# Kernel tuning notes

Hardware: AMD Instinct MI355X
Metric: run time of the kernel (lower is better)

Reference implementation:

```python
import jax, jax.numpy as jnp
import numpy as np
from jax import lax

B, L, C_IN = 8, 4096, 9
D_MODEL, D_STATE, D_CONV, EXPAND, N_LAYERS = 128, 16, 4, 2, 2
D_INNER = EXPAND * D_MODEL
DT_RANK = (D_MODEL + 15) // 16  # 8, mamba default ceil(d_model/16)


def setup_inputs() -> dict:
    key = jax.random.key(0)
    ks = jax.random.split(key, 8)
    s = 0.02
    A_log = jnp.log(jnp.broadcast_to(
        jnp.arange(1, D_STATE + 1, dtype=jnp.float32), (N_LAYERS, D_INNER, D_STATE)))
    return {
        "t": jax.random.normal(ks[0], (B, L, C_IN), jnp.float32),
        "emb_w": jax.random.normal(ks[1], (D_MODEL, C_IN, 3), jnp.float32) * s,
        "in_proj_w": jax.random.normal(ks[2], (N_LAYERS, 2 * D_INNER, D_MODEL), jnp.float32) * s,
        "conv_w": jax.random.normal(ks[3], (N_LAYERS, D_INNER, D_CONV), jnp.float32) * s,
        "conv_b": jnp.zeros((N_LAYERS, D_INNER), jnp.float32),
        "x_proj_w": jax.random.normal(ks[4], (N_LAYERS, DT_RANK + 2 * D_STATE, D_INNER), jnp.float32) * s,
        "dt_proj_w": jax.random.normal(ks[5], (N_LAYERS, D_INNER, DT_RANK), jnp.float32) * (DT_RANK ** -0.5),
        "dt_proj_b": jnp.full((N_LAYERS, D_INNER), -4.6, jnp.float32),  # softplus^-1(~0.01)
        "A_log": A_log,
        "D": jnp.ones((N_LAYERS, D_INNER), jnp.float32),
        "out_proj_w": jax.random.normal(ks[6], (N_LAYERS, D_MODEL, D_INNER), jnp.float32) * s,
    }


def token_embed(t, w):
    # circular-padded Conv1d(c_in -> d_model, kernel=3, padding=1, bias=False)
    Lt = t.shape[1]
    xp = jnp.pad(t, ((0, 0), (1, 1), (0, 0)), mode="wrap")  # (B, L+2, c_in)
    out = jnp.zeros((t.shape[0], Lt, w.shape[0]), t.dtype)
    for k in range(3):
        out = out + jnp.einsum("blc,dc->bld", xp[:, k:k + Lt], w[:, :, k])
    return out


def selective_scan(u, dt, A, Bm, Cm, Dv):
    # u, dt: (B,L,d_in); Bm, Cm: (B,L,d_state); A: (d_in,d_state); Dv: (d_in,)
    h0 = jnp.zeros((u.shape[0], u.shape[2], A.shape[1]), u.dtype)

    def step(h, xs):
        dt_i, b_i, c_i, u_i = xs  # (B,d_in), (B,ds), (B,ds), (B,d_in)
        dA = jnp.exp(dt_i[..., None] * A)                      # (B,d_in,ds)
        h = dA * h + (dt_i * u_i)[..., None] * b_i[:, None, :]  # (B,d_in,ds)
        y = jnp.einsum("bds,bs->bd", h, c_i)
        return h, y

    _, ys = lax.scan(step, h0, (dt.swapaxes(0, 1), Bm.swapaxes(0, 1),
                                 Cm.swapaxes(0, 1), u.swapaxes(0, 1)))
    return ys.swapaxes(0, 1) + u * Dv  # (B,L,d_in)


def mamba_block(x, in_w, cw, cb, xp_w, dtw, dtb, A_log, Dv, ow):
    Lt = x.shape[1]
    xz = jnp.einsum("bld,ed->ble", x, in_w)            # (B,L,2*d_inner)
    xc, z = jnp.split(xz, 2, axis=-1)
    # causal depthwise conv1d (kernel d_conv) + bias + silu
    xpad = jnp.pad(xc, ((0, 0), (D_CONV - 1, 0), (0, 0)))
    conv = cb
    acc = jnp.zeros_like(xc)
    for k in range(D_CONV):
        acc = acc + xpad[:, k:k + Lt] * cw[:, k]
    xc = jax.nn.silu(acc + cb)
    # input-dependent dt, B, C
    dbl = jnp.einsum("bld,rd->blr", xc, xp_w)           # (B,L,dt_rank+2*ds)
    dt = dbl[..., :DT_RANK]
    Bm = dbl[..., DT_RANK:DT_RANK + D_STATE]
    Cm = dbl[..., DT_RANK + D_STATE:]
    dt = jax.nn.softplus(jnp.einsum("blr,dr->bld", dt, dtw) + dtb)
    A = -jnp.exp(A_log)
    y = selective_scan(xc, dt, A, Bm, Cm, Dv)
    y = y * jax.nn.silu(z)
    return jnp.einsum("bld,md->blm", y, ow)             # (B,L,d_model)


def reference(t, emb_w, in_proj_w, conv_w, conv_b, x_proj_w, dt_proj_w,
              dt_proj_b, A_log, D, out_proj_w):
    x = token_embed(t, emb_w)
    for i in range(N_LAYERS):
        x = mamba_block(x, in_proj_w[i], conv_w[i], conv_b[i], x_proj_w[i],
                        dt_proj_w[i], dt_proj_b[i], A_log[i], D[i], out_proj_w[i])
    pooled = x.mean(axis=1)  # AdaptiveAvgPool1d(1) over time + flatten -> (B, d_model)
    nrm = jnp.maximum(jnp.linalg.norm(pooled, axis=1, keepdims=True), 1e-12)
    return pooled / nrm
```

## Files before the change

kernel.cpp:

```cpp
#include <hip/hip_runtime.h>
#include <cmath>

#define LOG2E 1.4426950408889634f
#define LN2   0.6931471805599453f

constexpr int Bb = 8;
constexpr int Ll = 4096;
constexpr int Mrows = Bb * Ll;
constexpr int NC = 128;
constexpr int CL = Ll / NC;

__device__ __forceinline__ float hexp2(float x) { return __builtin_amdgcn_exp2f(x); }
__device__ __forceinline__ float hlog2(float x) { return __builtin_amdgcn_logf(x); }
__device__ __forceinline__ float hrcp(float x)  { return __builtin_amdgcn_rcpf(x); }

__device__ __forceinline__ float softplus_f(float x) {
  const float t = hexp2(-fabsf(x) * LOG2E);
  return fmaxf(x, 0.f) + LN2 * hlog2(1.f + t);
}
__device__ __forceinline__ float sigmoid_f(float x) {
  return hrcp(1.f + hexp2(-x * LOG2E));
}

__global__ __launch_bounds__(128) void k_embed(const float* __restrict__ t,
                                               const float* __restrict__ w,
                                               float* __restrict__ x) {
  __shared__ float ws[128 * 27];
  const int d = threadIdx.x;
  for (int i = d; i < 128 * 27; i += 128) ws[i] = w[i];
  __syncthreads();
  const int bpb = Ll / 32;
  const int b = blockIdx.x / bpb;
  const int l0 = (blockIdx.x % bpb) * 32;
  const float* wd = &ws[d * 27];
  for (int l = l0; l < l0 + 32; ++l) {
    float acc = 0.f;
#pragma unroll
    for (int k = 0; k < 3; ++k) {
      int li = l + k - 1;
      if (li < 0) li += Ll;
      if (li >= Ll) li -= Ll;
      const float* tr = t + ((size_t)b * Ll + li) * 9;
#pragma unroll
      for (int c = 0; c < 9; ++c) acc = fmaf(tr[c], wd[c * 3 + k], acc);
    }
    x[((size_t)b * Ll + l) * 128 + d] = acc;
  }
}

template <int BM, int BN, int BK, int TM, int TN>
__global__ __launch_bounds__(256) void sgemm_tn(const float* __restrict__ A, int lda,
                                                const float* __restrict__ W, int ldw,
                                                float* __restrict__ C, int ldc,
                                                int N, int K) {
  constexpr int TX = BN / TN;
  constexpr int TY = BM / TM;
  static_assert(TX * TY == 256, "bad tile");
  __shared__ float As[BK][BM + 4];
  __shared__ float Bs[BK][BN + 4];
  const int m0 = blockIdx.x * BM;
  const int n0 = blockIdx.y * BN;
  const int tid = threadIdx.x;
  const int tx = tid % TX, ty = tid / TX;
  float acc[TM][TN];
#pragma unroll
  for (int i = 0; i < TM; ++i)
#pragma unroll
    for (int j = 0; j < TN; ++j) acc[i][j] = 0.f;

  constexpr int KV = BK / 4;
  const int lrow = tid / KV;
  const int lcol = (tid % KV) * 4;
  constexpr int RSTEP = 256 / KV;

  for (int k0 = 0; k0 < K; k0 += BK) {
#pragma unroll
    for (int r = lrow; r < BM; r += RSTEP) {
      float4 v = *(const float4*)(A + (size_t)(m0 + r) * lda + k0 + lcol);
      As[lcol + 0][r] = v.x; As[lcol + 1][r] = v.y;
      As[lcol + 2][r] = v.z; As[lcol + 3][r] = v.w;
    }
#pragma unroll
    for (int r = lrow; r < BN; r += RSTEP) {
      float4 v = make_float4(0.f, 0.f, 0.f, 0.f);
      if (n0 + r < N) v = *(const float4*)(W + (size_t)(n0 + r) * ldw + k0 + lcol);
      Bs[lcol + 0][r] = v.x; Bs[lcol + 1][r] = v.y;
      Bs[lcol + 2][r] = v.z; Bs[lcol + 3][r] = v.w;
    }
    __syncthreads();
#pragma unroll
    for (int k = 0; k < BK; ++k) {
      float ra[TM], rb[TN];
#pragma unroll
      for (int i = 0; i < TM; i += 4) {
        float4 v = *(const float4*)&As[k][ty * TM + i];
        ra[i + 0] = v.x; ra[i + 1] = v.y; ra[i + 2] = v.z; ra[i + 3] = v.w;
      }
#pragma unroll
      for (int j = 0; j < TN; j += 4) {
        float4 v = *(const float4*)&Bs[k][tx * TN + j];
        rb[j + 0] = v.x; rb[j + 1] = v.y; rb[j + 2] = v.z; rb[j + 3] = v.w;
      }
#pragma unroll
      for (int i = 0; i < TM; ++i)
#pragma unroll
        for (int j = 0; j < TN; ++j) acc[i][j] = fmaf(ra[i], rb[j], acc[i][j]);
    }
    __syncthreads();
  }
#pragma unroll
  for (int i = 0; i < TM; ++i) {
    const size_t row = (size_t)(m0 + ty * TM + i) * ldc + n0;
#pragma unroll
    for (int j = 0; j < TN; j += 4) {
      const int col = tx * TN + j;
      if (n0 + col < N) {
        float4 v = make_float4(acc[i][j], acc[i][j + 1], acc[i][j + 2], acc[i][j + 3]);
        *(float4*)(C + row + col) = v;
      }
    }
  }
}

__global__ __launch_bounds__(256) void k_conv_silu(const float* __restrict__ xz,
                                                   const float* __restrict__ cw,
                                                   const float* __restrict__ cb,
                                                   float* __restrict__ u) {
  const int idx = blockIdx.x * 256 + threadIdx.x;
  const int d = idx & 255;
  const int bl = idx >> 8;
  const int l = bl & (Ll - 1);
  const float4 wv = *(const float4*)(cw + d * 4);
  float acc = 0.f;
  if (l >= 3) {
    acc = fmaf(xz[((size_t)(bl - 3)) * 512 + d], wv.x, acc);
    acc = fmaf(xz[((size_t)(bl - 2)) * 512 + d], wv.y, acc);
    acc = fmaf(xz[((size_t)(bl - 1)) * 512 + d], wv.z, acc);
    acc = fmaf(xz[((size_t)(bl - 0)) * 512 + d], wv.w, acc);
  } else {
    if (l >= 2) acc = fmaf(xz[((size_t)(bl - 2)) * 512 + d], wv.y, acc);
    if (l >= 1) acc = fmaf(xz[((size_t)(bl - 1)) * 512 + d], wv.z, acc);
    acc = fmaf(xz[((size_t)bl) * 512 + d], wv.w, acc);
  }
  acc += cb[d];
  u[idx] = acc * sigmoid_f(acc);
}

#define LOAD_A2(base)                                                        \
  float4 a2a = *(const float4*)((base));                                     \
  float4 a2b = *(const float4*)((base) + 4);                                 \
  float4 a2c = *(const float4*)((base) + 8);                                 \
  float4 a2d = *(const float4*)((base) + 12);                                \
  a2a.x = -expf(a2a.x) * LOG2E; a2a.y = -expf(a2a.y) * LOG2E;                \
  a2a.z = -expf(a2a.z) * LOG2E; a2a.w = -expf(a2a.w) * LOG2E;                \
  a2b.x = -expf(a2b.x) * LOG2E; a2b.y = -expf(a2b.y) * LOG2E;                \
  a2b.z = -expf(a2b.z) * LOG2E; a2b.w = -expf(a2b.w) * LOG2E;                \
  a2c.x = -expf(a2c.x) * LOG2E; a2c.y = -expf(a2c.y) * LOG2E;                \
  a2c.z = -expf(a2c.z) * LOG2E; a2c.w = -expf(a2c.w) * LOG2E;                \
  a2d.x = -expf(a2d.x) * LOG2E; a2d.y = -expf(a2d.y) * LOG2E;                \
  a2d.z = -expf(a2d.z) * LOG2E; a2d.w = -expf(a2d.w) * LOG2E;

#define DT_FROM_Q(q0, q1, w0, w1, dtbv)                                      \
  float dtr = (dtbv);                                                        \
  dtr = fmaf((q0).x, (w0).x, dtr); dtr = fmaf((q0).y, (w0).y, dtr);          \
  dtr = fmaf((q0).z, (w0).z, dtr); dtr = fmaf((q0).w, (w0).w, dtr);          \
  dtr = fmaf((q1).x, (w1).x, dtr); dtr = fmaf((q1).y, (w1).y, dtr);          \
  dtr = fmaf((q1).z, (w1).z, dtr); dtr = fmaf((q1).w, (w1).w, dtr);

#define UPD1(H, A, Bv)                                                       \
  (H).x = fmaf(hexp2(sp * (A).x), (H).x, dtu * (Bv).x);                      \
  (H).y = fmaf(hexp2(sp * (A).y), (H).y, dtu * (Bv).y);                      \
  (H).z = fmaf(hexp2(sp * (A).z), (H).z, dtu * (Bv).z);                      \
  (H).w = fmaf(hexp2(sp * (A).w), (H).w, dtu * (Bv).w);

#define UPD3(H, A, Bv, Cv)                                                   \
  (H).x = fmaf(hexp2(sp * (A).x), (H).x, dtu * (Bv).x);                      \
  y = fmaf((H).x, (Cv).x, y);                                                \
  (H).y = fmaf(hexp2(sp * (A).y), (H).y, dtu * (Bv).y);                      \
  y = fmaf((H).y, (Cv).y, y);                                                \
  (H).z = fmaf(hexp2(sp * (A).z), (H).z, dtu * (Bv).z);                      \
  y = fmaf((H).z, (Cv).z, y);                                                \
  (H).w = fmaf(hexp2(sp * (A).w), (H).w, dtu * (Bv).w);                      \
  y = fmaf((H).w, (Cv).w, y);

__global__ __launch_bounds__(256) void k_scan_ph1(
    const float* __restrict__ u, const float* __restrict__ dbl,
    const float* __restrict__ dtw, const float* __restrict__ dtb,
    const float* __restrict__ alog, float* __restrict__ hloc,
    float* __restrict__ sdtc) {
  const int b = blockIdx.x / NC;
  const int c = blockIdx.x % NC;
  const int d = threadIdx.x;
  LOAD_A2(alog + d * 16)
  const float4 w0 = *(const float4*)(dtw + d * 8);
  const float4 w1 = *(const float4*)(dtw + d * 8 + 4);
  const float dtbv = dtb[d];
  float4 ha = make_float4(0.f, 0.f, 0.f, 0.f);
  float4 hb = ha, hc = ha, hd = ha;
  float sdt = 0.f;
  const float* ub = u + (size_t)b * Ll * 256 + d;
  const float* db = dbl + (size_t)b * Ll * 40;
  const int l0 = c * CL;
  for (int l = l0; l < l0 + CL; ++l) {
    const float uv = ub[(size_t)l * 256];
    const float* dr = db + (size_t)l * 40;
    const float4 q0 = *(const float4*)(dr);
    const float4 q1 = *(const float4*)(dr + 4);
    const float4 bfa = *(const float4*)(dr + 8);
    const float4 bfb = *(const float4*)(dr + 12);
    const float4 bfc = *(const float4*)(dr + 16);
    const float4 bfd = *(const float4*)(dr + 20);
    DT_FROM_Q(q0, q1, w0, w1, dtbv)
    const float sp = softplus_f(dtr);
    sdt += sp;
    const float dtu = sp * uv;
    UPD1(ha, a2a, bfa)
    UPD1(hb, a2b, bfb)
    UPD1(hc, a2c, bfc)
    UPD1(hd, a2d, bfd)
  }
  const size_t o = (size_t)(b * NC + c) * 256 + d;
  *(float4*)(hloc + o * 16 + 0)  = ha;
  *(float4*)(hloc + o * 16 + 4)  = hb;
  *(float4*)(hloc + o * 16 + 8)  = hc;
  *(float4*)(hloc + o * 16 + 12) = hd;
  sdtc[o] = sdt;
}

__global__ __launch_bounds__(256) void k_scan_ph2(
    const float* __restrict__ alog, const float* __restrict__ hloc,
    const float* __restrict__ sdtc, float* __restrict__ hstart) {
  const int b = blockIdx.x >> 4;
  const int dg = blockIdx.x & 15;
  const int d = dg * 16 + (threadIdx.x >> 4);
  const int s = threadIdx.x & 15;
  const float A2 = -expf(alog[d * 16 + s]) * LOG2E;
  float hs = 0.f;
  for (int c = 0; c < NC; ++c) {
    const size_t o = (size_t)(b * NC + c) * 256 + d;
    hstart[o * 16 + s] = hs;
    const float sdt = sdtc[o];
    hs = fmaf(hexp2(A2 * sdt), hs, hloc[o * 16 + s]);
  }
}

__global__ __launch_bounds__(256) void k_scan_ph3(
    const float* __restrict__ u, const float* __restrict__ dbl,
    const float* __restrict__ dtw, const float* __restrict__ dtb,
    const float* __restrict__ alog, const float* __restrict__ Dv,
    const float* __restrict__ hstart, float* __restrict__ xz) {
  const int b = blockIdx.x / NC;
  const int c = blockIdx.x % NC;
  const int d = threadIdx.x;
  LOAD_A2(alog + d * 16)
  const float4 w0 = *(const float4*)(dtw + d * 8);
  const float4 w1 = *(const float4*)(dtw + d * 8 + 4);
  const float dtbv = dtb[d];
  const float Dd = Dv[d];
  const size_t o = (size_t)(b * NC + c) * 256 + d;
  float4 ha = *(const float4*)(hstart + o * 16 + 0);
  float4 hb = *(const float4*)(hstart + o * 16 + 4);
  float4 hc = *(const float4*)(hstart + o * 16 + 8);
  float4 hd = *(const float4*)(hstart + o * 16 + 12);
  const float* ub = u + (size_t)b * Ll * 256 + d;
  const float* db = dbl + (size_t)b * Ll * 40;
  const int l0 = c * CL;
  for (int l = l0; l < l0 + CL; ++l) {
    const float uv = ub[(size_t)l * 256];
    const float* dr = db + (size_t)l * 40;
    const float4 q0 = *(const float4*)(dr);
    const float4 q1 = *(const float4*)(dr + 4);
    const float4 bfa = *(const float4*)(dr + 8);
    const float4 bfb = *(const float4*)(dr + 12);
    const float4 bfc = *(const float4*)(dr + 16);
    const float4 bfd = *(const float4*)(dr + 20);
    const float4 cfa = *(const float4*)(dr + 24);
    const float4 cfb = *(const float4*)(dr + 28);
    const float4 cfc = *(const float4*)(dr + 32);
    const float4 cfd = *(const float4*)(dr + 36);
    DT_FROM_Q(q0, q1, w0, w1, dtbv)
    const float sp = softplus_f(dtr);
    const float dtu = sp * uv;
    float y = 0.f;
    UPD3(ha, a2a, bfa, cfa)
    UPD3(hb, a2b, bfb, cfb)
    UPD3(hc, a2c, bfc, cfc)
    UPD3(hd, a2d, bfd, cfd)
    y = fmaf(uv, Dd, y);
    const size_t row = ((size_t)b * Ll + l) * 512;
    const float zv = xz[row + 256 + d];
    xz[row + d] = y * (zv * sigmoid_f(zv));
  }
}

__global__ __launch_bounds__(128) void k_pool_part(const float* __restrict__ x,
                                                   float* __restrict__ part) {
  const int b = blockIdx.x >> 5;
  const int c = blockIdx.x & 31;
  const int m = threadIdx.x;
  const float* xb = x + (size_t)b * Ll * 128 + (size_t)c * 128 * 128 + m;
  float s = 0.f;
#pragma unroll 4
  for (int l = 0; l < 128; ++l) s += xb[(size_t)l * 128];
  part[(size_t)blockIdx.x * 128 + m] = s;
}

__global__ __launch_bounds__(128) void k_pool_fin(const float* __restrict__ part,
                                                  float* __restrict__ out) {
  const int b = blockIdx.x, m = threadIdx.x;
  float p = 0.f;
#pragma unroll
  for (int c = 0; c < 32; ++c) p += part[((size_t)b * 32 + c) * 128 + m];
  p *= (1.f / Ll);
  __shared__ float pm[128];
  __shared__ float sq[128];
  pm[m] = p;
  sq[m] = p * p;
  __syncthreads();
  for (int wd = 64; wd >= 1; wd >>= 1) {
    if (m < wd) sq[m] += sq[m + wd];
    __syncthreads();
  }
  out[b * 128 + m] = pm[m] / fmaxf(sqrtf(sq[0]), 1e-12f);
}

extern "C" void kernel_launch(void* const* d_in, const int* in_sizes, int n_in,
                              void* d_out, int out_size, void* d_ws, size_t ws_size,
                              hipStream_t stream) {
  (void)in_sizes; (void)n_in; (void)out_size; (void)ws_size;
  const float* t    = (const float*)d_in[0];
  const float* embw = (const float*)d_in[1];
  const float* inw  = (const float*)d_in[2];
  const float* cw   = (const float*)d_in[3];
  const float* cb   = (const float*)d_in[4];
  const float* xpw  = (const float*)d_in[5];
  const float* dtw  = (const float*)d_in[6];
  const float* dtb  = (const float*)d_in[7];
  const float* alog = (const float*)d_in[8];
  const float* Dv   = (const float*)d_in[9];
  const float* ow   = (const float*)d_in[10];

  float* wsf  = (float*)d_ws;
  float* xz   = wsf;
  float* xb   = xz + 16777216;
  float* ubuf = xb + 4194304;
  float* dblb = ubuf + 8388608;
  float* hloc = dblb + 1310720;
  float* hst  = hloc + 4194304;
  float* sdtc = hst + 4194304;
  float* pool = sdtc + 262144;
  float* outp = (float*)d_out;

  k_embed<<<dim3(Bb * (Ll / 32)), dim3(128), 0, stream>>>(t, embw, xb);

  for (int layer = 0; layer < 2; ++layer) {
    const float* inw_l = inw + (size_t)layer * 512 * 128;
    const float* cw_l  = cw + layer * 256 * 4;
    const float* cb_l  = cb + layer * 256;
    const float* xpw_l = xpw + layer * 40 * 256;
    const float* dtw_l = dtw + layer * 256 * 8;
    const float* dtb_l = dtb + layer * 256;
    const float* al_l  = alog + layer * 256 * 16;
    const float* D_l   = Dv + layer * 256;
    const float* ow_l  = ow + layer * 128 * 256;

    sgemm_tn<128, 128, 32, 8, 8><<<dim3(Mrows / 128, 4), 256, 0, stream>>>(
        xb, 128, inw_l, 128, xz, 512, 512, 128);
    k_conv_silu<<<dim3(Mrows), 256, 0, stream>>>(xz, cw_l, cb_l, ubuf);
    sgemm_tn<64, 64, 32, 4, 4><<<dim3(Mrows / 64, 1), 256, 0, stream>>>(
        ubuf, 256, xpw_l, 256, dblb, 40, 40, 256);
    k_scan_ph1<<<dim3(Bb * NC), 256, 0, stream>>>(ubuf, dblb, dtw_l, dtb_l, al_l, hloc, sdtc);
    k_scan_ph2<<<dim3(Bb * 16), 256, 0, stream>>>(al_l, hloc, sdtc, hst);
    k_scan_ph3<<<dim3(Bb * NC), 256, 0, stream>>>(ubuf, dblb, dtw_l, dtb_l, al_l, D_l, hst, xz);
    sgemm_tn<64, 128, 32, 4, 8><<<dim3(Mrows / 64, 1), 256, 0, stream>>>(
        xz, 512, ow_l, 256, xb, 128, 128, 256);
  }

  k_pool_part<<<dim3(Bb * 32), 128, 0, stream>>>(xb, pool);
  k_pool_fin<<<dim3(Bb), 128, 0, stream>>>(pool, outp);
}
```

Before: 479.7 us.

## Replace FP32 SIMT GEMMs with split-bf16 triple-MFMA GEMMs and drop hstart buffer

Replaces the three fp32 SIMT sgemm calls with an MFMA kernel that splits each fp32 operand into three bf16 pieces (hi/mid/lo) and combines six bf16 MFMAs to emulate near-fp32 accuracy. Weights are pre-split by new kernels on each call, and activations are split in-kernel while staging to LDS. The scan phase 2 now writes chunk start states in place into hloc, removing the separate hstart buffer. This trades more MFMA issues and split arithmetic for higher matrix throughput, and takes a small accuracy risk from the bf16 decomposition.

```diff
diff --git a/kernel.cpp b/kernel.cpp
--- a/kernel.cpp
+++ b/kernel.cpp
@@ -3,6 +3,7 @@
 
 #define LOG2E 1.4426950408889634f
 #define LN2   0.6931471805599453f
+#define C8    0.00390625f
 
 constexpr int Bb = 8;
 constexpr int Ll = 4096;
@@ -10,6 +11,10 @@
 constexpr int NC = 128;
 constexpr int CL = Ll / NC;
 
+typedef unsigned short u16;
+typedef short s16x8 __attribute__((ext_vector_type(8)));
+typedef float f32x4 __attribute__((ext_vector_type(4)));
+
 __device__ __forceinline__ float hexp2(float x) { return __builtin_amdgcn_exp2f(x); }
 __device__ __forceinline__ float hlog2(float x) { return __builtin_amdgcn_logf(x); }
 __device__ __forceinline__ float hrcp(float x)  { return __builtin_amdgcn_rcpf(x); }
@@ -20,6 +25,38 @@
 }
 __device__ __forceinline__ float sigmoid_f(float x) {
   return hrcp(1.f + hexp2(-x * LOG2E));
+}
+
+__device__ __forceinline__ f32x4 mfma_bf(s16x8 a, s16x8 b, f32x4 c) {
+  return __builtin_amdgcn_mfma_f32_16x16x32_bf16(a, b, c, 0, 0, 0);
+}
+
+__device__ __forceinline__ u16 bf16rne(float v) {
+  unsigned u = __float_as_uint(v);
+  u += 0x7FFFu + ((u >> 16) & 1u);
+  return (u16)(u >> 16);
+}
+__device__ __forceinline__ float bf2f(u16 h) {
+  return __uint_as_float(((unsigned)h) << 16);
+}
+__device__ __forceinline__ void split3(float v, u16& h, u16& m, u16& l) {
+  h = bf16rne(v);
+  const float r1 = (v - bf2f(h)) * 256.f;
+  m = bf16rne(r1);
+  const float r2 = (r1 - bf2f(m)) * 256.f;
+  l = bf16rne(r2);
+}
+
+__global__ __launch_bounds__(256) void k_split3(const float* __restrict__ src,
+                                                u16* __restrict__ h,
+                                                u16* __restrict__ m,
+                                                u16* __restrict__ l, int n) {
+  const int i = blockIdx.x * 256 + threadIdx.x;
+  if (i < n) {
+    u16 a, b, c;
+    split3(src[i], a, b, c);
+    h[i] = a; m[i] = b; l[i] = c;
+  }
 }
 
 __global__ __launch_bounds__(128) void k_embed(const float* __restrict__ t,
@@ -48,75 +85,101 @@
   }
 }
 
-template <int BM, int BN, int BK, int TM, int TN>
-__global__ __launch_bounds__(256) void sgemm_tn(const float* __restrict__ A, int lda,
-                                                const float* __restrict__ W, int ldw,
-                                                float* __restrict__ C, int ldc,
-                                                int N, int K) {
-  constexpr int TX = BN / TN;
-  constexpr int TY = BM / TM;
-  static_assert(TX * TY == 256, "bad tile");
-  __shared__ float As[BK][BM + 4];
-  __shared__ float Bs[BK][BN + 4];
-  const int m0 = blockIdx.x * BM;
-  const int n0 = blockIdx.y * BN;
+__global__ __launch_bounds__(512) void gemm3s(
+    const float* __restrict__ A, int lda,
+    const u16* __restrict__ Wh, const u16* __restrict__ Wm,
+    const u16* __restrict__ Wl,
+    float* __restrict__ C, int ldc, int N, int K) {
+  __shared__ __align__(16) u16 Lh[128 * 40];
+  __shared__ __align__(16) u16 Lm[128 * 40];
+  __shared__ __align__(16) u16 Ll2[128 * 40];
+  const int m0 = blockIdx.x * 128;
+  const int n0 = blockIdx.y * 128;
   const int tid = threadIdx.x;
-  const int tx = tid % TX, ty = tid / TX;
-  float acc[TM][TN];
-#pragma unroll
-  for (int i = 0; i < TM; ++i)
-#pragma unroll
-    for (int j = 0; j < TN; ++j) acc[i][j] = 0.f;
-
-  constexpr int KV = BK / 4;
-  const int lrow = tid / KV;
-  const int lcol = (tid % KV) * 4;
-  constexpr int RSTEP = 256 / KV;
-
-  for (int k0 = 0; k0 < K; k0 += BK) {
-#pragma unroll
-    for (int r = lrow; r < BM; r += RSTEP) {
-      float4 v = *(const float4*)(A + (size_t)(m0 + r) * lda + k0 + lcol);
-      As[lcol + 0][r] = v.x; As[lcol + 1][r] = v.y;
-      As[lcol + 2][r] = v.z; As[lcol + 3][r] = v.w;
+  const int lane = tid & 63;
+  const int wid = tid >> 6;
+  const int wm = wid & 1;
+  const int wn = wid >> 1;
+  const int lr = lane & 15;
+  const int lq = lane >> 4;
+
+  f32x4 a0[4][2], a1[4][2], a2[4][2];
+  const f32x4 zz = {0.f, 0.f, 0.f, 0.f};
+#pragma unroll
+  for (int i = 0; i < 4; ++i)
+#pragma unroll
+    for (int j = 0; j < 2; ++j) { a0[i][j] = zz; a1[i][j] = zz; a2[i][j] = zz; }
+
+  const int col0 = n0 + wn * 32 + lr;
+  const int col1 = col0 + 16;
+  const int c0 = col0 < N ? col0 : N - 1;
+  const int c1 = col1 < N ? col1 : N - 1;
+  const size_t bo0 = (size_t)c0 * K + lq * 8;
+  const size_t bo1 = (size_t)c1 * K + lq * 8;
+
+  const int srow = tid >> 2;
+  const int sg = (tid & 3) * 8;
+  const float* pa = A + (size_t)(m0 + srow) * lda + sg;
+  const int sdst = srow * 40 + sg;
+
+  for (int k0 = 0; k0 < K; k0 += 32) {
+    const float4 va = *(const float4*)(pa + k0);
+    const float4 vb = *(const float4*)(pa + k0 + 4);
+    s16x8 h8, m8, l8;
+    {
+      u16 h, m, l;
+      split3(va.x, h, m, l); h8[0] = (short)h; m8[0] = (short)m; l8[0] = (short)l;
+      split3(va.y, h, m, l); h8[1] = (short)h; m8[1] = (short)m; l8[1] = (short)l;
+      split3(va.z, h, m, l); h8[2] = (short)h; m8[2] = (short)m; l8[2] = (short)l;
+      split3(va.w, h, m, l); h8[3] = (short)h; m8[3] = (short)m; l8[3] = (short)l;
+      split3(vb.x, h, m, l); h8[4] = (short)h; m8[4] = (short)m; l8[4] = (short)l;
+      split3(vb.y, h, m, l); h8[5] = (short)h; m8[5] = (short)m; l8[5] = (short)l;
+      split3(vb.z, h, m, l); h8[6] = (short)h; m8[6] = (short)m; l8[6] = (short)l;
+      split3(vb.w, h, m, l); h8[7] = (short)h; m8[7] = (short)m; l8[7] = (short)l;
     }
-#pragma unroll
-    for (int r = lrow; r < BN; r += RSTEP) {
-      float4 v = make_float4(0.f, 0.f, 0.f, 0.f);
-      if (n0 + r < N) v = *(const float4*)(W + (size_t)(n0 + r) * ldw + k0 + lcol);
-      Bs[lcol + 0][r] = v.x; Bs[lcol + 1][r] = v.y;
-      Bs[lcol + 2][r] = v.z; Bs[lcol + 3][r] = v.w;
+    *(s16x8*)&Lh[sdst] = h8;
+    *(s16x8*)&Lm[sdst] = m8;
+    *(s16x8*)&Ll2[sdst] = l8;
+    __syncthreads();
+    const s16x8 bh0 = *(const s16x8*)(Wh + bo0 + k0);
+    const s16x8 bh1 = *(const s16x8*)(Wh + bo1 + k0);
+    const s16x8 bm0 = *(const s16x8*)(Wm + bo0 + k0);
+    const s16x8 bm1 = *(const s16x8*)(Wm + bo1 + k0);
+    const s16x8 bl0 = *(const s16x8*)(Wl + bo0 + k0);
+    const s16x8 bl1 = *(const s16x8*)(Wl + bo1 + k0);
+#pragma unroll
+    for (int mf = 0; mf < 4; ++mf) {
+      const int ar = (wm * 64 + mf * 16 + lr) * 40 + lq * 8;
+      const s16x8 ah = *(const s16x8*)&Lh[ar];
+      const s16x8 am = *(const s16x8*)&Lm[ar];
+      const s16x8 al = *(const s16x8*)&Ll2[ar];
+      a0[mf][0] = mfma_bf(ah, bh0, a0[mf][0]);
+      a1[mf][0] = mfma_bf(ah, bm0, a1[mf][0]);
+      a1[mf][0] = mfma_bf(am, bh0, a1[mf][0]);
+      a2[mf][0] = mfma_bf(ah, bl0, a2[mf][0]);
+      a2[mf][0] = mfma_bf(al, bh0, a2[mf][0]);
+      a2[mf][0] = mfma_bf(am, bm0, a2[mf][0]);
+      a0[mf][1] = mfma_bf(ah, bh1, a0[mf][1]);
+      a1[mf][1] = mfma_bf(ah, bm1, a1[mf][1]);
+      a1[mf][1] = mfma_bf(am, bh1, a1[mf][1]);
+      a2[mf][1] = mfma_bf(ah, bl1, a2[mf][1]);
+      a2[mf][1] = mfma_bf(al, bh1, a2[mf][1]);
+      a2[mf][1] = mfma_bf(am, bm1, a2[mf][1]);
     }
     __syncthreads();
-#pragma unroll
-    for (int k = 0; k < BK; ++k) {
-      float ra[TM], rb[TN];
-#pragma unroll
-      for (int i = 0; i < TM; i += 4) {
-        float4 v = *(const float4*)&As[k][ty * TM + i];
-        ra[i + 0] = v.x; ra[i + 1] = v.y; ra[i + 2] = v.z; ra[i + 3] = v.w;
-      }
-#pragma unroll
-      for (int j = 0; j < TN; j += 4) {
-        float4 v = *(const float4*)&Bs[k][tx * TN + j];
-        rb[j + 0] = v.x; rb[j + 1] = v.y; rb[j + 2] = v.z; rb[j + 3] = v.w;
-      }
-#pragma unroll
-      for (int i = 0; i < TM; ++i)
-#pragma unroll
-        for (int j = 0; j < TN; ++j) acc[i][j] = fmaf(ra[i], rb[j], acc[i][j]);
-    }
-    __syncthreads();
-  }
-#pragma unroll
-  for (int i = 0; i < TM; ++i) {
-    const size_t row = (size_t)(m0 + ty * TM + i) * ldc + n0;
-#pragma unroll
-    for (int j = 0; j < TN; j += 4) {
-      const int col = tx * TN + j;
-      if (n0 + col < N) {
-        float4 v = make_float4(acc[i][j], acc[i][j + 1], acc[i][j + 2], acc[i][j + 3]);
-        *(float4*)(C + row + col) = v;
+  }
+#pragma unroll
+  for (int mf = 0; mf < 4; ++mf) {
+#pragma unroll
+    for (int nf = 0; nf < 2; ++nf) {
+      const int col = n0 + wn * 32 + nf * 16 + lr;
+      if (col < N) {
+#pragma unroll
+        for (int r = 0; r < 4; ++r) {
+          const int row = m0 + wm * 64 + mf * 16 + lq * 4 + r;
+          C[(size_t)row * ldc + col] =
+              fmaf(C8, fmaf(C8, a2[mf][nf][r], a1[mf][nf][r]), a0[mf][nf][r]);
+        }
       }
     }
   }
@@ -228,8 +291,8 @@
 }
 
 __global__ __launch_bounds__(256) void k_scan_ph2(
-    const float* __restrict__ alog, const float* __restrict__ hloc,
-    const float* __restrict__ sdtc, float* __restrict__ hstart) {
+    const float* __restrict__ alog, float* __restrict__ hloc,
+    const float* __restrict__ sdtc) {
   const int b = blockIdx.x >> 4;
   const int dg = blockIdx.x & 15;
   const int d = dg * 16 + (threadIdx.x >> 4);
@@ -238,9 +301,9 @@
   float hs = 0.f;
   for (int c = 0; c < NC; ++c) {
     const size_t o = (size_t)(b * NC + c) * 256 + d;
-    hstart[o * 16 + s] = hs;
-    const float sdt = sdtc[o];
-    hs = fmaf(hexp2(A2 * sdt), hs, hloc[o * 16 + s]);
+    const float tmp = hloc[o * 16 + s];
+    hloc[o * 16 + s] = hs;
+    hs = fmaf(hexp2(A2 * sdtc[o]), hs, tmp);
   }
 }
 
@@ -346,34 +409,55 @@
   float* ubuf = xb + 4194304;
   float* dblb = ubuf + 8388608;
   float* hloc = dblb + 1310720;
-  float* hst  = hloc + 4194304;
-  float* sdtc = hst + 4194304;
+  float* sdtc = hloc + 4194304;
   float* pool = sdtc + 262144;
+  float* wtb  = pool + 32768;
+  u16* wih = (u16*)(wtb);
+  u16* wim = (u16*)(wtb + 65536);
+  u16* wil = (u16*)(wtb + 131072);
+  u16* wxh = (u16*)(wtb + 196608);
+  u16* wxm = (u16*)(wtb + 206848);
+  u16* wxl = (u16*)(wtb + 217088);
+  u16* woh = (u16*)(wtb + 227328);
+  u16* wom = (u16*)(wtb + 260096);
+  u16* wol = (u16*)(wtb + 292864);
   float* outp = (float*)d_out;
 
+  k_split3<<<dim3(512), 256, 0, stream>>>(inw, wih, wim, wil, 131072);
+  k_split3<<<dim3(80),  256, 0, stream>>>(xpw, wxh, wxm, wxl, 20480);
+  k_split3<<<dim3(256), 256, 0, stream>>>(ow,  woh, wom, wol, 65536);
+
   k_embed<<<dim3(Bb * (Ll / 32)), dim3(128), 0, stream>>>(t, embw, xb);
 
   for (int layer = 0; layer < 2; ++layer) {
-    const float* inw_l = inw + (size_t)layer * 512 * 128;
+    const u16* wih_l = wih + (size_t)layer * 512 * 128;
+    const u16* wim_l = wim + (size_t)layer * 512 * 128;
+    const u16* wil_l = wil + (size_t)layer * 512 * 128;
+    const u16* wxh_l = wxh + (size_t)layer * 40 * 256;
+    const u16* wxm_l = wxm + (size_t)layer * 40 * 256;
+    const u16* wxl_l = wxl + (size_t)layer * 40 * 256;
+    const u16* woh_l = woh + (size_t)layer * 128 * 256;
+    const u16* wom_l = wom + (size_t)layer * 128 * 256;
+    const u16* wol_l = wol + (size_t)layer * 128 * 256;
     const float* cw_l  = cw + layer * 256 * 4;
     const float* cb_l  = cb + layer * 256;
-    const float* xpw_l = xpw + layer * 40 * 256;
     const float* dtw_l = dtw + layer * 256 * 8;
     const float* dtb_l = dtb + layer * 256;
     const float* al_l  = alog + layer * 256 * 16;
     const float* D_l   = Dv + layer * 256;
-    const float* ow_l  = ow + layer * 128 * 256;
-
-    sgemm_tn<128, 128, 32, 8, 8><<<dim3(Mrows / 128, 4), 256, 0, stream>>>(
-        xb, 128, inw_l, 128, xz, 512, 512, 128);
+
+    gemm3s<<<dim3(Mrows / 128, 4), 512, 0, stream>>>(
+        xb, 128, wih_l, wim_l, wil_l, xz, 512, 512, 128);
     k_conv_silu<<<dim3(Mrows), 256, 0, stream>>>(xz, cw_l, cb_l, ubuf);
-    sgemm_tn<64, 64, 32, 4, 4><<<dim3(Mrows / 64, 1), 256, 0, stream>>>(
-        ubuf, 256, xpw_l, 256, dblb, 40, 40, 256);
-    k_scan_ph1<<<dim3(Bb * NC), 256, 0, stream>>>(ubuf, dblb, dtw_l, dtb_l, al_l, hloc, sdtc);
-    k_scan_ph2<<<dim3(Bb * 16), 256, 0, stream>>>(al_l, hloc, sdtc, hst);
-    k_scan_ph3<<<dim3(Bb * NC), 256, 0, stream>>>(ubuf, dblb, dtw_l, dtb_l, al_l, D_l, hst, xz);
-    sgemm_tn<64, 128, 32, 4, 8><<<dim3(Mrows / 64, 1), 256, 0, stream>>>(
-        xz, 512, ow_l, 256, xb, 128, 128, 256);
+    gemm3s<<<dim3(Mrows / 128, 1), 512, 0, stream>>>(
+        ubuf, 256, wxh_l, wxm_l, wxl_l, dblb, 40, 40, 256);
+    k_scan_ph1<<<dim3(Bb * NC), 256, 0, stream>>>(ubuf, dblb, dtw_l, dtb_l,
+                                                  al_l, hloc, sdtc);
+    k_scan_ph2<<<dim3(Bb * 16), 256, 0, stream>>>(al_l, hloc, sdtc);
+    k_scan_ph3<<<dim3(Bb * NC), 256, 0, stream>>>(ubuf, dblb, dtw_l, dtb_l,
+                                                  al_l, D_l, hloc, xz);
+    gemm3s<<<dim3(Mrows / 128, 1), 512, 0, stream>>>(
+        xz, 512, woh_l, wom_l, wol_l, xb, 128, 128, 256);
   }
 
   k_pool_part<<<dim3(Bb * 32), 128, 0, stream>>>(xb, pool);
```

Result: faster. 454.8 us (-5.2%).
